# Optimization experiments

Hardware: AMD Instinct MI355X
Metric: run time of the kernel (lower is better)

Reference implementation:

```python
import jax, jax.numpy as jnp
import numpy as np

E, H, D, FF, DEC, K, PAD = 20, 5, 4, 120, 40, 50, 25

def make_pe(embed_size, L):
    # faithful to the odd PositionalEncoding loop: even rows use exponent 2*i/E,
    # odd rows use exponent 2*(i+1)/E
    pos = np.arange(L, dtype=np.float64)[None, :]
    i = np.arange(0, embed_size, 2, dtype=np.float64)[:, None]
    pe = np.zeros((embed_size, L), dtype=np.float32)
    pe[0::2] = np.sin(pos / 10000.0 ** (2.0 * i / embed_size))
    pe[1::2] = np.cos(pos / 10000.0 ** (2.0 * (i + 1.0) / embed_size))
    return pe

def layernorm(x, g, b, eps=1e-5):
    mu = jnp.mean(x, axis=-1, keepdims=True)
    var = jnp.mean(jnp.square(x - mu), axis=-1, keepdims=True)
    return (x - mu) * jax.lax.rsqrt(var + eps) * g + b

def setup_inputs() -> dict:
    key = jax.random.key(0)
    ks = jax.random.split(key, 32)
    n = lambda k, s: jax.random.normal(k, s, dtype=jnp.float32) * 0.05
    inp = {
        'x': jax.random.normal(ks[0], (2, 5000), dtype=jnp.float32),
        'conv_w': n(ks[1], (E, 1, K)),
        # 4 transformer blocks, params stacked on leading axis
        'Wv': n(ks[2], (4, D, D)), 'Wk': n(ks[3], (4, D, D)), 'Wq': n(ks[4], (4, D, D)),
        'Wc': n(ks[5], (4, E, E)), 'bc': n(ks[6], (4, E)),
        'lnA_g': jnp.ones((4, E), jnp.float32), 'lnA_b': jnp.zeros((4, E), jnp.float32),
        'W1': n(ks[7], (4, FF, E)), 'b1': n(ks[8], (4, FF)),
        'W2': n(ks[9], (4, E, FF)), 'b2': n(ks[10], (4, E)),
        'lnB_g': jnp.ones((4, E), jnp.float32), 'lnB_b': jnp.zeros((4, E), jnp.float32),
        # MLP decoder
        'f1_w': n(ks[11], (DEC, E)), 'f1_b': n(ks[12], (DEC,)),
        'f2_w': n(ks[13], (DEC, DEC)), 'f2_b': n(ks[14], (DEC,)),
        'f3_w': n(ks[15], (E, DEC)), 'f3_b': n(ks[16], (E,)),
        'f4_w': n(ks[17], (1, E)), 'f4_b': n(ks[18], (1,)),
    }
    return inp

def reference(x, conv_w, Wv, Wk, Wq, Wc, bc, lnA_g, lnA_b, W1, b1, W2, b2,
              lnB_g, lnB_b, f1_w, f1_b, f2_w, f2_b, f3_w, f3_b, f4_w, f4_b):
    B, L = x.shape
    # conv embed: (B,1,L) -> (B,E,L+1) -> slice to L
    out = jax.lax.conv_general_dilated(
        x[:, None, :], conv_w, window_strides=(1,), padding=[(PAD, PAD)],
        dimension_numbers=('NCW', 'OIW', 'NCW'))[:, :, :L]
    out = out + jnp.asarray(make_pe(E, L))[None]          # pos encoding
    h = jnp.transpose(out, (0, 2, 1))                      # (B,L,E)
    scale = 1.0 / np.sqrt(float(E))                        # NOTE: sqrt(embed_size), not sqrt(head_dim)
    for i in range(4):
        s = h.reshape(B, L, H, D)                          # (B,L,H,D)
        v = s @ Wv[i].T
        k = s @ Wk[i].T
        q = s @ Wq[i].T
        att = jax.nn.softmax(jnp.einsum('nqhd,nkhd->nhqk', q, k) * scale, axis=-1)
        o = jnp.einsum('nhql,nlhd->nqhd', att, v).reshape(B, L, E)
        o = o @ Wc[i].T + bc[i]
        h1 = layernorm(o + h, lnA_g[i], lnA_b[i])
        fw = jax.nn.relu(h1 @ W1[i].T + b1[i]) @ W2[i].T + b2[i]
        h = layernorm(fw + h1, lnB_g[i], lnB_b[i])
    d = jax.nn.relu(h @ f1_w.T + f1_b)
    d = jax.nn.relu(d @ f2_w.T + f2_b)
    d = jax.nn.relu(d @ f3_w.T + f3_b)
    return jax.nn.sigmoid(d @ f4_w.T + f4_b)               # (B,L,1)
```

## Files before the change

### kernel.cpp

```cpp
#include <hip/hip_runtime.h>
#include <math.h>

#define B_ 2
#define L_ 5000
#define E_ 20
#define H_ 5
#define FF_ 120
#define DEC_ 40
#define K_ 50
#define PAD_ 25
#define SCALE 0.22360679774997896f

#define NM 35
#define MST2 180
#define MLAYER (B_ * H_ * MST2)
#define ACH 128
#define NCH 40

typedef float v2f __attribute__((ext_vector_type(2)));
__device__ __forceinline__ v2f vsplat(float x) { v2f r; r.x = x; r.y = x; return r; }

__constant__ int TD[NM] = {4, 0,1,2,3, 0,0,0,0,1,1,1,2,2,3,
                           0,0,0,0,0,0,0,0,0,0,1,1,1,1,1,1,2,2,2,3};
__constant__ int TE[NM] = {4, 4,4,4,4, 0,1,2,3,1,2,3,2,3,3,
                           0,0,0,0,1,1,1,2,2,3,1,1,1,2,2,3,2,2,3,3};
__constant__ int TF[NM] = {4, 4,4,4,4, 4,4,4,4,4,4,4,4,4,4,
                           0,1,2,3,1,2,3,2,3,3,1,2,3,2,3,3,2,3,3,3};

__device__ __forceinline__ void mono36(const float x[4], float m[36]) {
  int idx = 0;
  m[idx++] = 1.f;
#pragma unroll
  for (int d = 0; d < 4; d++) m[idx++] = x[d];
#pragma unroll
  for (int d = 0; d < 4; d++)
#pragma unroll
    for (int e = d; e < 4; e++) m[idx++] = x[d] * x[e];
#pragma unroll
  for (int d = 0; d < 4; d++)
#pragma unroll
    for (int e = d; e < 4; e++)
#pragma unroll
      for (int f = e; f < 4; f++) m[idx++] = x[d] * x[e] * x[f];
  m[35] = 0.f;
}

__device__ __forceinline__ void qcoef(float* mq) {
  const float S = 1.f / 6.f;
  mq[5]  *= 0.5f; mq[9]  *= 0.5f; mq[12] *= 0.5f; mq[14] *= 0.5f;
  mq[15] *= S;    mq[25] *= S;    mq[31] *= S;    mq[34] *= S;
  mq[16] *= 0.5f; mq[17] *= 0.5f; mq[18] *= 0.5f; mq[19] *= 0.5f;
  mq[22] *= 0.5f; mq[24] *= 0.5f; mq[26] *= 0.5f; mq[27] *= 0.5f;
  mq[28] *= 0.5f; mq[30] *= 0.5f; mq[32] *= 0.5f; mq[33] *= 0.5f;
}

__global__ __launch_bounds__(256) void conv_pe_kernel(
    const float* __restrict__ x, const float* __restrict__ w,
    float* __restrict__ hbuf, float* __restrict__ Mall) {
  int tid = blockIdx.x * 256 + threadIdx.x;
  if (tid < 4 * MLAYER) Mall[tid] = 0.f;
  if (tid >= B_ * L_ * E_) return;
  int e = tid % E_;
  int bl = tid / E_;
  int b = bl / L_, l = bl % L_;

  const float* xr = x + b * L_;
  const float* wr = w + e * K_;
  float a0 = 0.f, a1 = 0.f;
#pragma unroll
  for (int k = 0; k < K_; k += 2) {
    int i0 = l + k - PAD_, i1 = i0 + 1;
    float x0 = (i0 >= 0 && i0 < L_) ? xr[i0] : 0.f;
    float x1 = (i1 >= 0 && i1 < L_) ? xr[i1] : 0.f;
    a0 += x0 * wr[k];
    a1 += x1 * wr[k + 1];
  }
  double expo = (e & 1) ? (double)(e + 1) / (double)E_ : (double)e / (double)E_;
  double factor = pow(10000.0, -expo);
  double arg = (double)l * factor;
  float pe = (e & 1) ? (float)cos(arg) : (float)sin(arg);
  hbuf[bl * E_ + e] = (a0 + a1) + pe;
}

__global__ __launch_bounds__(192, 1) void moment_kernel(
    const float* __restrict__ hbuf,
    const float* __restrict__ Wk, const float* __restrict__ Wv,
    const float* __restrict__ W2, float* __restrict__ W2t,
    float* __restrict__ M) {
  __shared__ __align__(16) float kvs[10][ACH + 2];
  int bh = blockIdx.x / NCH;
  int chunk = blockIdx.x % NCH;
  int b = bh / H_, hh = bh % H_;

  if (blockIdx.x == 0) {
    for (int i = threadIdx.x; i < E_ * FF_; i += 192) {
      int e = i / FF_, j = i % FF_;
      W2t[j * E_ + e] = W2[i];
    }
  }

  if (threadIdx.x < ACH) {
    float wk[16], wv[16];
#pragma unroll
    for (int i = 0; i < 16; i++) { wk[i] = Wk[i]; wv[i] = Wv[i]; }
    int j = chunk * ACH + threadIdx.x;
    bool valid = j < L_;
    int jc = valid ? j : (L_ - 1);
    float4 s4 = *(const float4*)(hbuf + (b * L_ + jc) * E_ + hh * 4);
    float vm = valid ? 1.f : 0.f;
    int t = threadIdx.x;
    kvs[0][t] = wk[0] * s4.x + wk[1] * s4.y + wk[2] * s4.z + wk[3] * s4.w;
    kvs[1][t] = wk[4] * s4.x + wk[5] * s4.y + wk[6] * s4.z + wk[7] * s4.w;
    kvs[2][t] = wk[8] * s4.x + wk[9] * s4.y + wk[10] * s4.z + wk[11] * s4.w;
    kvs[3][t] = wk[12] * s4.x + wk[13] * s4.y + wk[14] * s4.z + wk[15] * s4.w;
    kvs[4][t] = 1.f;
    kvs[5][t] = (wv[0] * s4.x + wv[1] * s4.y + wv[2] * s4.z + wv[3] * s4.w) * vm;
    kvs[6][t] = (wv[4] * s4.x + wv[5] * s4.y + wv[6] * s4.z + wv[7] * s4.w) * vm;
    kvs[7][t] = (wv[8] * s4.x + wv[9] * s4.y + wv[10] * s4.z + wv[11] * s4.w) * vm;
    kvs[8][t] = (wv[12] * s4.x + wv[13] * s4.y + wv[14] * s4.z + wv[15] * s4.w) * vm;
    kvs[9][t] = vm;
  }
  __syncthreads();

  int t = threadIdx.x;
  if (t >= NM * 5) return;
  int m = t / 5, c = t % 5;
  int sd = TD[m], se = TE[m], sf = TF[m], sv = 5 + c;
  v2f acc = vsplat(0.f);
#pragma unroll 4
  for (int j = 0; j < ACH; j += 2) {
    v2f a = *(const v2f*)&kvs[sd][j];
    v2f bq = *(const v2f*)&kvs[se][j];
    v2f cq = *(const v2f*)&kvs[sf][j];
    v2f vv = *(const v2f*)&kvs[sv][j];
    acc += a * bq * cq * vv;
  }
  atomicAdd(&M[bh * MST2 + c * 36 + m], acc.x + acc.y);
}

#define DOT20G(res, W, row, vec)                                     \
  {                                                                  \
    const float4* Wr = (const float4*)((W) + (row) * 20);            \
    float c0 = 0.f, c1 = 0.f, c2 = 0.f, c3 = 0.f;                    \
    _Pragma("unroll") for (int g5 = 0; g5 < 5; g5++) {               \
      float4 w4 = Wr[g5];                                            \
      c0 += w4.x * vec[g5 * 4 + 0];                                  \
      c1 += w4.y * vec[g5 * 4 + 1];                                  \
      c2 += w4.z * vec[g5 * 4 + 2];                                  \
      c3 += w4.w * vec[g5 * 4 + 3];                                  \
    }                                                                \
    res += (c0 + c1) + (c2 + c3);                                    \
  }

#define DOT40G(res, W, row, vec)                                     \
  {                                                                  \
    const float4* Wr = (const float4*)((W) + (row) * 40);            \
    float c0 = 0.f, c1 = 0.f, c2 = 0.f, c3 = 0.f;                    \
    _Pragma("unroll") for (int g5 = 0; g5 < 10; g5++) {              \
      float4 w4 = Wr[g5];                                            \
      c0 += w4.x * vec[g5 * 4 + 0];                                  \
      c1 += w4.y * vec[g5 * 4 + 1];                                  \
      c2 += w4.z * vec[g5 * 4 + 2];                                  \
      c3 += w4.w * vec[g5 * 4 + 3];                                  \
    }                                                                \
    res += (c0 + c1) + (c2 + c3);                                    \
  }

template <int LAST>
__global__ __launch_bounds__(128) void fused_kernel(
    const float* __restrict__ M, const float* __restrict__ Wq,
    const float* __restrict__ Wc, const float* __restrict__ bc,
    const float* __restrict__ lnAg, const float* __restrict__ lnAb,
    const float* __restrict__ W1, const float* __restrict__ b1,
    const float* __restrict__ W2t, const float* __restrict__ b2,
    const float* __restrict__ lnBg, const float* __restrict__ lnBb,
    float* __restrict__ hbuf,
    const float* __restrict__ f1w, const float* __restrict__ f1b,
    const float* __restrict__ f2w, const float* __restrict__ f2b,
    const float* __restrict__ f3w, const float* __restrict__ f3b,
    const float* __restrict__ f4w, const float* __restrict__ f4b,
    float* __restrict__ out) {
  __shared__ __align__(16) float4 so4[16][7];
  __shared__ __align__(16) float stv[16 * 20];
  __shared__ __align__(16) float sc[128 * 20];

  int tid = threadIdx.x;
  int b = blockIdx.y;
  int p16 = tid & 15;
  int part = tid >> 4;
  int l = blockIdx.x * 16 + p16;
  bool act = l < L_;
  int lc = act ? l : L_ - 1;
  int pos = b * L_ + lc;

  float hv[E_];
#pragma unroll
  for (int e4 = 0; e4 < 5; e4++) {
    float4 h4 = *(const float4*)(hbuf + pos * E_ + e4 * 4);
    hv[e4 * 4 + 0] = h4.x; hv[e4 * 4 + 1] = h4.y;
    hv[e4 * 4 + 2] = h4.z; hv[e4 * 4 + 3] = h4.w;
  }

  if (part < H_) {
    float4 qsrc = *(const float4*)(hbuf + pos * E_ + part * 4);
    float q[4];
#pragma unroll
    for (int d = 0; d < 4; d++) {
      q[d] = (Wq[d * 4 + 0] * qsrc.x + Wq[d * 4 + 1] * qsrc.y +
              Wq[d * 4 + 2] * qsrc.z + Wq[d * 4 + 3] * qsrc.w) *
             SCALE;
    }
    float mq[36];
    mono36(q, mq);
    qcoef(mq);
    const float* Mb = M + (b * H_ + part) * MST2;
    float oc[5];
#pragma unroll
    for (int c = 0; c < 5; c++) {
      const float4* Mr = (const float4*)(Mb + c * 36);
      float a0 = 0.f, a1 = 0.f, a2 = 0.f, a3 = 0.f;
#pragma unroll
      for (int g = 0; g < 9; g++) {
        float4 w4 = Mr[g];
        a0 += w4.x * mq[g * 4 + 0];
        a1 += w4.y * mq[g * 4 + 1];
        a2 += w4.z * mq[g * 4 + 2];
        a3 += w4.w * mq[g * 4 + 3];
      }
      oc[c] = (a0 + a1) + (a2 + a3);
    }
    float inv = 1.f / oc[4];
    so4[p16][part] =
        make_float4(oc[0] * inv, oc[1] * inv, oc[2] * inv, oc[3] * inv);
  }
  __syncthreads();

  float o[E_];
#pragma unroll
  for (int hh = 0; hh < H_; hh++) {
    float4 o4 = so4[p16][hh];
    o[hh * 4 + 0] = o4.x; o[hh * 4 + 1] = o4.y;
    o[hh * 4 + 2] = o4.z; o[hh * 4 + 3] = o4.w;
  }
  int r0 = (part < 4) ? part * 3 : 12 + (part - 4) * 2;
  int nr = (part < 4) ? 3 : 2;
  for (int r = 0; r < nr; r++) {
    int row = r0 + r;
    float acc = bc[row];
    DOT20G(acc, Wc, row, o);
    stv[p16 * 20 + row] = acc;
  }
  __syncthreads();

  float tv[E_];
#pragma unroll
  for (int e4 = 0; e4 < 5; e4++) {
    float4 t4 = *(const float4*)(stv + p16 * 20 + e4 * 4);
    tv[e4 * 4 + 0] = t4.x + hv[e4 * 4 + 0];
    tv[e4 * 4 + 1] = t4.y + hv[e4 * 4 + 1];
    tv[e4 * 4 + 2] = t4.z + hv[e4 * 4 + 2];
    tv[e4 * 4 + 3] = t4.w + hv[e4 * 4 + 3];
  }
  float mu = 0.f;
#pragma unroll
  for (int e = 0; e < E_; e++) mu += tv[e];
  mu *= (1.f / E_);
  float var = 0.f;
#pragma unroll
  for (int e = 0; e < E_; e++) { float d = tv[e] - mu; var += d * d; }
  var *= (1.f / E_);
  float rs = rsqrtf(var + 1e-5f);
  float h1[E_];
#pragma unroll
  for (int e = 0; e < E_; e++) h1[e] = (tv[e] - mu) * rs * lnAg[e] + lnAb[e];

  float g2p[E_];
#pragma unroll
  for (int e = 0; e < E_; e++) g2p[e] = 0.f;
  int jf0 = part * (FF_ / 8);
#pragma unroll
  for (int jj = 0; jj < FF_ / 8; jj++) {
    int j = jf0 + jj;
    float f = b1[j];
    DOT20G(f, W1, j, h1);
    f = fmaxf(f, 0.f);
    const float4* Wr = (const float4*)(W2t + j * 20);
#pragma unroll
    for (int g = 0; g < 5; g++) {
      float4 w4 = Wr[g];
      g2p[g * 4 + 0] += w4.x * f;
      g2p[g * 4 + 1] += w4.y * f;
      g2p[g * 4 + 2] += w4.z * f;
      g2p[g * 4 + 3] += w4.w * f;
    }
  }
  float4* scw = (float4*)(sc + tid * 20);
#pragma unroll
  for (int g = 0; g < 5; g++)
    scw[g] = make_float4(g2p[g * 4], g2p[g * 4 + 1], g2p[g * 4 + 2],
                         g2p[g * 4 + 3]);
  __syncthreads();

  float g2[E_];
#pragma unroll
  for (int e = 0; e < E_; e++) g2[e] = b2[e] + h1[e];
#pragma unroll
  for (int pp = 0; pp < 8; pp++) {
    const float4* r = (const float4*)(sc + (pp * 16 + p16) * 20);
#pragma unroll
    for (int g = 0; g < 5; g++) {
      float4 v4 = r[g];
      g2[g * 4 + 0] += v4.x; g2[g * 4 + 1] += v4.y;
      g2[g * 4 + 2] += v4.z; g2[g * 4 + 3] += v4.w;
    }
  }
  float mu2 = 0.f;
#pragma unroll
  for (int e = 0; e < E_; e++) mu2 += g2[e];
  mu2 *= (1.f / E_);
  float var2 = 0.f;
#pragma unroll
  for (int e = 0; e < E_; e++) { float d = g2[e] - mu2; var2 += d * d; }
  var2 *= (1.f / E_);
  float rs2 = rsqrtf(var2 + 1e-5f);
  float hn[E_];
#pragma unroll
  for (int e = 0; e < E_; e++) hn[e] = (g2[e] - mu2) * rs2 * lnBg[e] + lnBb[e];

  if (!LAST) {
    if (act && part == 0) {
#pragma unroll
      for (int e4 = 0; e4 < 5; e4++) {
        *(float4*)(hbuf + pos * E_ + e4 * 4) =
            make_float4(hn[e4 * 4], hn[e4 * 4 + 1], hn[e4 * 4 + 2],
                        hn[e4 * 4 + 3]);
      }
    }
  } else {
    __syncthreads();
#pragma unroll
    for (int j = 0; j < DEC_ / 8; j++) {
      int jj = part * (DEC_ / 8) + j;
      float a = f1b[jj];
      DOT20G(a, f1w, jj, hn);
      sc[p16 * 101 + jj] = fmaxf(a, 0.f);
    }
    __syncthreads();
    float d1[DEC_];
#pragma unroll
    for (int k = 0; k < DEC_; k++) d1[k] = sc[p16 * 101 + k];
#pragma unroll
    for (int j = 0; j < DEC_ / 8; j++) {
      int jj = part * (DEC_ / 8) + j;
      float a = f2b[jj];
      DOT40G(a, f2w, jj, d1);
      sc[p16 * 101 + 40 + jj] = fmaxf(a, 0.f);
    }
    __syncthreads();
    float d2[DEC_];
#pragma unroll
    for (int k = 0; k < DEC_; k++) d2[k] = sc[p16 * 101 + 40 + k];
    if (part < 5) {
#pragma unroll
      for (int j = 0; j < 4; j++) {
        int ee = part * 4 + j;
        float a = f3b[ee];
        DOT40G(a, f3w, ee, d2);
        sc[p16 * 101 + 80 + ee] = fmaxf(a, 0.f);
      }
    }
    __syncthreads();
    if (act && part == 0) {
      float z = f4b[0];
      const float* dv = sc + p16 * 101 + 80;
      DOT20G(z, f4w, 0, dv);
      out[pos] = 1.f / (1.f + __expf(-z));
    }
  }
}

extern "C" void kernel_launch(void* const* d_in, const int* in_sizes, int n_in,
                              void* d_out, int out_size, void* d_ws,
                              size_t ws_size, hipStream_t stream) {
  const float* x    = (const float*)d_in[0];
  const float* cw   = (const float*)d_in[1];
  const float* Wv   = (const float*)d_in[2];
  const float* Wk   = (const float*)d_in[3];
  const float* Wq   = (const float*)d_in[4];
  const float* Wc   = (const float*)d_in[5];
  const float* bc   = (const float*)d_in[6];
  const float* lnAg = (const float*)d_in[7];
  const float* lnAb = (const float*)d_in[8];
  const float* W1   = (const float*)d_in[9];
  const float* b1   = (const float*)d_in[10];
  const float* W2   = (const float*)d_in[11];
  const float* b2   = (const float*)d_in[12];
  const float* lnBg = (const float*)d_in[13];
  const float* lnBb = (const float*)d_in[14];
  const float* f1w  = (const float*)d_in[15];
  const float* f1b  = (const float*)d_in[16];
  const float* f2w  = (const float*)d_in[17];
  const float* f2b  = (const float*)d_in[18];
  const float* f3w  = (const float*)d_in[19];
  const float* f3b  = (const float*)d_in[20];
  const float* f4w  = (const float*)d_in[21];
  const float* f4b  = (const float*)d_in[22];
  float* out = (float*)d_out;

  float* ws = (float*)d_ws;
  float* h = ws;
  float* Mall = ws + 200000;
  float* W2t = Mall + 4 * MLAYER;

  conv_pe_kernel<<<(B_ * L_ * E_ + 255) / 256, 256, 0, stream>>>(x, cw, h, Mall);

  for (int i = 0; i < 4; i++) {
    moment_kernel<<<B_ * H_ * NCH, 192, 0, stream>>>(
        h, Wk + i * 16, Wv + i * 16, W2 + i * 2400, W2t, Mall + i * MLAYER);
    dim3 grid((L_ + 15) / 16, B_);
    if (i < 3) {
      fused_kernel<0><<<grid, 128, 0, stream>>>(
          Mall + i * MLAYER, Wq + i * 16, Wc + i * 400, bc + i * 20,
          lnAg + i * 20, lnAb + i * 20, W1 + i * 2400, b1 + i * 120,
          W2t, b2 + i * 20, lnBg + i * 20, lnBb + i * 20, h,
          f1w, f1b, f2w, f2b, f3w, f3b, f4w, f4b, out);
    } else {
      fused_kernel<1><<<grid, 128, 0, stream>>>(
          Mall + i * MLAYER, Wq + i * 16, Wc + i * 400, bc + i * 20,
          lnAg + i * 20, lnAb + i * 20, W1 + i * 2400, b1 + i * 120,
          W2t, b2 + i * 20, lnBg + i * 20, lnBb + i * 20, h,
          f1w, f1b, f2w, f2b, f3w, f3b, f4w, f4b, out);
    }
  }
}
```

Before: 196.3 us.

## Fuse attention moment accumulation into producer kernels with deterministic two-stage reduction

Drops the separate moment_kernel. The per-position K/V polynomial moment partials are now computed inside the conv/PE kernel for layer 0 and inside the fused layer kernel for the next layer, each writing per-block partials to a buffer. A small mreduce kernel then sums those partials, replacing global atomics and avoiding a re-read of hbuf. All four W2 transposes are also done once up front. In exchange, every block does extra shared-memory work and writes a large partial buffer, and one tiny reduction launch is added per layer.

```diff
diff --git a/kernel.cpp b/kernel.cpp
--- a/kernel.cpp
+++ b/kernel.cpp
@@ -11,21 +11,9 @@
 #define PAD_ 25
 #define SCALE 0.22360679774997896f
 
-#define NM 35
-#define MST2 180
-#define MLAYER (B_ * H_ * MST2)
-#define ACH 128
-#define NCH 40
-
-typedef float v2f __attribute__((ext_vector_type(2)));
-__device__ __forceinline__ v2f vsplat(float x) { v2f r; r.x = x; r.y = x; return r; }
-
-__constant__ int TD[NM] = {4, 0,1,2,3, 0,0,0,0,1,1,1,2,2,3,
-                           0,0,0,0,0,0,0,0,0,0,1,1,1,1,1,1,2,2,2,3};
-__constant__ int TE[NM] = {4, 4,4,4,4, 0,1,2,3,1,2,3,2,3,3,
-                           0,0,0,0,1,1,1,2,2,3,1,1,1,2,2,3,2,2,3,3};
-__constant__ int TF[NM] = {4, 4,4,4,4, 4,4,4,4,4,4,4,4,4,4,
-                           0,1,2,3,1,2,3,2,3,3,1,2,3,2,3,3,2,3,3,3};
+#define NBX 313
+#define COLP 320
+#define NSLOT 900
 
 __device__ __forceinline__ void mono36(const float x[4], float m[36]) {
   int idx = 0;
@@ -54,88 +42,117 @@
   mq[28] *= 0.5f; mq[30] *= 0.5f; mq[32] *= 0.5f; mq[33] *= 0.5f;
 }
 
+__device__ __forceinline__ void kv_partials(
+    const float* sh21, const float* __restrict__ Wk,
+    const float* __restrict__ Wv, int p16, int hh, float msk,
+    float* smono, float* sv) {
+  float s0 = sh21[p16 * 21 + hh * 4 + 0];
+  float s1 = sh21[p16 * 21 + hh * 4 + 1];
+  float s2 = sh21[p16 * 21 + hh * 4 + 2];
+  float s3 = sh21[p16 * 21 + hh * 4 + 3];
+  float kk[4], vk[4];
+#pragma unroll
+  for (int d = 0; d < 4; d++) {
+    kk[d] = Wk[d * 4 + 0] * s0 + Wk[d * 4 + 1] * s1 + Wk[d * 4 + 2] * s2 +
+            Wk[d * 4 + 3] * s3;
+    vk[d] = (Wv[d * 4 + 0] * s0 + Wv[d * 4 + 1] * s1 + Wv[d * 4 + 2] * s2 +
+             Wv[d * 4 + 3] * s3) * msk;
+  }
+  float mm[36];
+  mono36(kk, mm);
+#pragma unroll
+  for (int m = 0; m < 36; m++) smono[(hh * 36 + m) * 20 + p16] = mm[m];
+#pragma unroll
+  for (int c = 0; c < 4; c++) sv[(hh * 5 + c) * 20 + p16] = vk[c];
+  sv[(hh * 5 + 4) * 20 + p16] = msk;
+}
+
+__device__ __forceinline__ void slot_reduce_store(
+    const float* smono, const float* sv, int tid, int tcount, int b, int bx,
+    float* __restrict__ Mpart) {
+  for (int s = tid; s < NSLOT; s += tcount) {
+    int hh = s / 180, r = s % 180, c = r / 36, m = r % 36;
+    const float4* A = (const float4*)(smono + (hh * 36 + m) * 20);
+    const float4* V = (const float4*)(sv + (hh * 5 + c) * 20);
+    float a0 = 0.f, a1 = 0.f, a2 = 0.f, a3 = 0.f;
+#pragma unroll
+    for (int g = 0; g < 4; g++) {
+      float4 av = A[g];
+      float4 vv = V[g];
+      a0 += av.x * vv.x; a1 += av.y * vv.y;
+      a2 += av.z * vv.z; a3 += av.w * vv.w;
+    }
+    Mpart[(b * NSLOT + s) * COLP + bx] = (a0 + a1) + (a2 + a3);
+  }
+}
+
 __global__ __launch_bounds__(256) void conv_pe_kernel(
-    const float* __restrict__ x, const float* __restrict__ w,
-    float* __restrict__ hbuf, float* __restrict__ Mall) {
-  int tid = blockIdx.x * 256 + threadIdx.x;
-  if (tid < 4 * MLAYER) Mall[tid] = 0.f;
-  if (tid >= B_ * L_ * E_) return;
-  int e = tid % E_;
-  int bl = tid / E_;
-  int b = bl / L_, l = bl % L_;
-
-  const float* xr = x + b * L_;
-  const float* wr = w + e * K_;
-  float a0 = 0.f, a1 = 0.f;
-#pragma unroll
-  for (int k = 0; k < K_; k += 2) {
-    int i0 = l + k - PAD_, i1 = i0 + 1;
-    float x0 = (i0 >= 0 && i0 < L_) ? xr[i0] : 0.f;
-    float x1 = (i1 >= 0 && i1 < L_) ? xr[i1] : 0.f;
-    a0 += x0 * wr[k];
-    a1 += x1 * wr[k + 1];
-  }
-  double expo = (e & 1) ? (double)(e + 1) / (double)E_ : (double)e / (double)E_;
-  double factor = pow(10000.0, -expo);
-  double arg = (double)l * factor;
-  float pe = (e & 1) ? (float)cos(arg) : (float)sin(arg);
-  hbuf[bl * E_ + e] = (a0 + a1) + pe;
-}
-
-__global__ __launch_bounds__(192, 1) void moment_kernel(
-    const float* __restrict__ hbuf,
+    const float* __restrict__ x, const float* __restrict__ cw,
     const float* __restrict__ Wk, const float* __restrict__ Wv,
-    const float* __restrict__ W2, float* __restrict__ W2t,
-    float* __restrict__ M) {
-  __shared__ __align__(16) float kvs[10][ACH + 2];
-  int bh = blockIdx.x / NCH;
-  int chunk = blockIdx.x % NCH;
-  int b = bh / H_, hh = bh % H_;
-
-  if (blockIdx.x == 0) {
-    for (int i = threadIdx.x; i < E_ * FF_; i += 192) {
-      int e = i / FF_, j = i % FF_;
-      W2t[j * E_ + e] = W2[i];
-    }
-  }
-
-  if (threadIdx.x < ACH) {
-    float wk[16], wv[16];
-#pragma unroll
-    for (int i = 0; i < 16; i++) { wk[i] = Wk[i]; wv[i] = Wv[i]; }
-    int j = chunk * ACH + threadIdx.x;
-    bool valid = j < L_;
-    int jc = valid ? j : (L_ - 1);
-    float4 s4 = *(const float4*)(hbuf + (b * L_ + jc) * E_ + hh * 4);
-    float vm = valid ? 1.f : 0.f;
-    int t = threadIdx.x;
-    kvs[0][t] = wk[0] * s4.x + wk[1] * s4.y + wk[2] * s4.z + wk[3] * s4.w;
-    kvs[1][t] = wk[4] * s4.x + wk[5] * s4.y + wk[6] * s4.z + wk[7] * s4.w;
-    kvs[2][t] = wk[8] * s4.x + wk[9] * s4.y + wk[10] * s4.z + wk[11] * s4.w;
-    kvs[3][t] = wk[12] * s4.x + wk[13] * s4.y + wk[14] * s4.z + wk[15] * s4.w;
-    kvs[4][t] = 1.f;
-    kvs[5][t] = (wv[0] * s4.x + wv[1] * s4.y + wv[2] * s4.z + wv[3] * s4.w) * vm;
-    kvs[6][t] = (wv[4] * s4.x + wv[5] * s4.y + wv[6] * s4.z + wv[7] * s4.w) * vm;
-    kvs[7][t] = (wv[8] * s4.x + wv[9] * s4.y + wv[10] * s4.z + wv[11] * s4.w) * vm;
-    kvs[8][t] = (wv[12] * s4.x + wv[13] * s4.y + wv[14] * s4.z + wv[15] * s4.w) * vm;
-    kvs[9][t] = vm;
-  }
-  __syncthreads();
-
-  int t = threadIdx.x;
-  if (t >= NM * 5) return;
-  int m = t / 5, c = t % 5;
-  int sd = TD[m], se = TE[m], sf = TF[m], sv = 5 + c;
-  v2f acc = vsplat(0.f);
-#pragma unroll 4
-  for (int j = 0; j < ACH; j += 2) {
-    v2f a = *(const v2f*)&kvs[sd][j];
-    v2f bq = *(const v2f*)&kvs[se][j];
-    v2f cq = *(const v2f*)&kvs[sf][j];
-    v2f vv = *(const v2f*)&kvs[sv][j];
-    acc += a * bq * cq * vv;
-  }
-  atomicAdd(&M[bh * MST2 + c * 36 + m], acc.x + acc.y);
+    const float* __restrict__ W2, float* __restrict__ hbuf,
+    float* __restrict__ W2t, float* __restrict__ Mpart0) {
+  __shared__ float sx[68];
+  __shared__ float sh[16 * 21];
+  __shared__ __align__(16) float smono[H_ * 36 * 20];
+  __shared__ __align__(16) float sv[H_ * 5 * 20];
+
+  int tid = threadIdx.x;
+  int bx = blockIdx.x, b = blockIdx.y;
+  int l0 = bx * 16;
+
+  if (bx == 0 && b == 0) {
+    for (int i = tid; i < 4 * E_ * FF_; i += 256) {
+      int layer = i / (E_ * FF_), r = i % (E_ * FF_);
+      int e = r / FF_, j = r % FF_;
+      W2t[layer * 2400 + j * E_ + e] = W2[i];
+    }
+  }
+  if (tid < 65) {
+    int xi = l0 - PAD_ + tid;
+    sx[tid] = (xi >= 0 && xi < L_) ? x[b * L_ + xi] : 0.f;
+  }
+  __syncthreads();
+
+  for (int item = tid; item < 16 * E_; item += 256) {
+    int pi = item / E_, e = item % E_;
+    const float* wr = cw + e * K_;
+    float a0 = 0.f, a1 = 0.f;
+#pragma unroll
+    for (int k = 0; k < K_; k += 2) {
+      a0 += sx[pi + k] * wr[k];
+      a1 += sx[pi + k + 1] * wr[k + 1];
+    }
+    double expo = (e & 1) ? (double)(e + 1) / 20.0 : (double)e / 20.0;
+    double factor = pow(10000.0, -expo);
+    double arg = (double)(l0 + pi) * factor;
+    float pe = (e & 1) ? (float)cos(arg) : (float)sin(arg);
+    float hval = (a0 + a1) + pe;
+    sh[pi * 21 + e] = hval;
+    if (l0 + pi < L_) hbuf[((size_t)b * L_ + l0 + pi) * E_ + e] = hval;
+  }
+  __syncthreads();
+
+  if (tid < 16 * H_) {
+    int p16 = tid & 15, hh = tid >> 4;
+    float msk = (l0 + p16 < L_) ? 1.f : 0.f;
+    kv_partials(sh, Wk, Wv, p16, hh, msk, smono, sv);
+  }
+  __syncthreads();
+  slot_reduce_store(smono, sv, tid, 256, b, bx, Mpart0);
+}
+
+__global__ __launch_bounds__(256) void mreduce_kernel(
+    const float* __restrict__ Mpart, float* __restrict__ M) {
+  int g = blockIdx.x * 256 + threadIdx.x;
+  if (g >= B_ * NSLOT) return;
+  const float* base = Mpart + (size_t)g * COLP;
+  const float4* bp = (const float4*)base;
+  float a0 = 0.f, a1 = 0.f, a2 = 0.f, a3 = 0.f;
+  for (int q = 0; q < 78; q++) {
+    float4 v = bp[q];
+    a0 += v.x; a1 += v.y; a2 += v.z; a3 += v.w;
+  }
+  M[g] = (a0 + a1) + (a2 + a3) + base[312];
 }
 
 #define DOT20G(res, W, row, vec)                                     \
@@ -175,6 +192,8 @@
     const float* __restrict__ W2t, const float* __restrict__ b2,
     const float* __restrict__ lnBg, const float* __restrict__ lnBb,
     float* __restrict__ hbuf,
+    const float* __restrict__ Wk2, const float* __restrict__ Wv2,
+    float* __restrict__ Mpn,
     const float* __restrict__ f1w, const float* __restrict__ f1b,
     const float* __restrict__ f2w, const float* __restrict__ f2b,
     const float* __restrict__ f3w, const float* __restrict__ f3b,
@@ -183,6 +202,9 @@
   __shared__ __align__(16) float4 so4[16][7];
   __shared__ __align__(16) float stv[16 * 20];
   __shared__ __align__(16) float sc[128 * 20];
+  __shared__ float ssh[LAST ? 4 : 16 * 21];
+  __shared__ __align__(16) float smono[LAST ? 4 : H_ * 36 * 20];
+  __shared__ __align__(16) float sv[LAST ? 4 : H_ * 5 * 20];
 
   int tid = threadIdx.x;
   int b = blockIdx.y;
@@ -213,7 +235,7 @@
     float mq[36];
     mono36(q, mq);
     qcoef(mq);
-    const float* Mb = M + (b * H_ + part) * MST2;
+    const float* Mb = M + b * NSLOT + part * 180;
     float oc[5];
 #pragma unroll
     for (int c = 0; c < 5; c++) {
@@ -328,14 +350,25 @@
   for (int e = 0; e < E_; e++) hn[e] = (g2[e] - mu2) * rs2 * lnBg[e] + lnBb[e];
 
   if (!LAST) {
-    if (act && part == 0) {
-#pragma unroll
-      for (int e4 = 0; e4 < 5; e4++) {
-        *(float4*)(hbuf + pos * E_ + e4 * 4) =
-            make_float4(hn[e4 * 4], hn[e4 * 4 + 1], hn[e4 * 4 + 2],
-                        hn[e4 * 4 + 3]);
+    if (part == 0) {
+      if (act) {
+#pragma unroll
+        for (int e4 = 0; e4 < 5; e4++) {
+          *(float4*)(hbuf + pos * E_ + e4 * 4) =
+              make_float4(hn[e4 * 4], hn[e4 * 4 + 1], hn[e4 * 4 + 2],
+                          hn[e4 * 4 + 3]);
+        }
       }
-    }
+#pragma unroll
+      for (int e = 0; e < E_; e++) ssh[p16 * 21 + e] = hn[e];
+    }
+    __syncthreads();
+    if (part < H_) {
+      float msk = act ? 1.f : 0.f;
+      kv_partials(ssh, Wk2, Wv2, p16, part, msk, smono, sv);
+    }
+    __syncthreads();
+    slot_reduce_store(smono, sv, tid, 128, b, (int)blockIdx.x, Mpn);
   } else {
     __syncthreads();
 #pragma unroll
@@ -409,26 +442,30 @@
 
   float* ws = (float*)d_ws;
   float* h = ws;
-  float* Mall = ws + 200000;
-  float* W2t = Mall + 4 * MLAYER;
-
-  conv_pe_kernel<<<(B_ * L_ * E_ + 255) / 256, 256, 0, stream>>>(x, cw, h, Mall);
+  float* M = ws + 200000;
+  float* W2t = M + B_ * NSLOT;
+  float* Mp0 = W2t + 4 * 2400;
+  float* Mp1 = Mp0 + (size_t)B_ * NSLOT * COLP;
+  float* Mp[2] = {Mp0, Mp1};
+
+  dim3 grid(NBX, B_);
+  conv_pe_kernel<<<grid, 256, 0, stream>>>(x, cw, Wk, Wv, W2, h, W2t, Mp0);
 
   for (int i = 0; i < 4; i++) {
-    moment_kernel<<<B_ * H_ * NCH, 192, 0, stream>>>(
-        h, Wk + i * 16, Wv + i * 16, W2 + i * 2400, W2t, Mall + i * MLAYER);
-    dim3 grid((L_ + 15) / 16, B_);
+    mreduce_kernel<<<(B_ * NSLOT + 255) / 256, 256, 0, stream>>>(Mp[i & 1], M);
     if (i < 3) {
       fused_kernel<0><<<grid, 128, 0, stream>>>(
-          Mall + i * MLAYER, Wq + i * 16, Wc + i * 400, bc + i * 20,
-          lnAg + i * 20, lnAb + i * 20, W1 + i * 2400, b1 + i * 120,
-          W2t, b2 + i * 20, lnBg + i * 20, lnBb + i * 20, h,
+          M, Wq + i * 16, Wc + i * 400, bc + i * 20, lnAg + i * 20,
+          lnAb + i * 20, W1 + i * 2400, b1 + i * 120, W2t + i * 2400,
+          b2 + i * 20, lnBg + i * 20, lnBb + i * 20, h,
+          Wk + (i + 1) * 16, Wv + (i + 1) * 16, Mp[(i + 1) & 1],
           f1w, f1b, f2w, f2b, f3w, f3b, f4w, f4b, out);
     } else {
       fused_kernel<1><<<grid, 128, 0, stream>>>(
-          Mall + i * MLAYER, Wq + i * 16, Wc + i * 400, bc + i * 20,
-          lnAg + i * 20, lnAb + i * 20, W1 + i * 2400, b1 + i * 120,
-          W2t, b2 + i * 20, lnBg + i * 20, lnBb + i * 20, h,
+          M, Wq + i * 16, Wc + i * 400, bc + i * 20, lnAg + i * 20,
+          lnAb + i * 20, W1 + i * 2400, b1 + i * 120, W2t + i * 2400,
+          b2 + i * 20, lnBg + i * 20, lnBb + i * 20, h,
+          Wk, Wv, Mp0,
           f1w, f1b, f2w, f2b, f3w, f3b, f4w, f4b, out);
     }
   }
```

Measured after the change: 230.2 us. +17.3%, slower.
